# Kernel optimization log

Hardware: AMD Instinct MI355X
Metric: run time of the kernel (lower is better)

The kernel has to match this reference:

```python
import jax, jax.numpy as jnp
import numpy as np

N = 50000          # nodes
E = 1_600_000      # edges (avg degree 32)
F_IN = 48          # node features (df columns 1:-1)
H, C = 8, 8        # conv1: 8 heads x 8 channels
NC = 2             # num_classes
NEG_SLOPE = 0.2    # PyG GATConv default leaky_relu slope


def setup_inputs() -> dict:
    key = jax.random.key(0)
    ks = jax.random.split(key, 9)
    s = 0.1
    return {
        "x": jax.random.normal(ks[0], (N, F_IN), jnp.float32),
        "edge_index": jax.random.randint(ks[1], (2, E), 0, N, dtype=jnp.int64),
        "W1": jax.random.normal(ks[2], (F_IN, H * C), jnp.float32) * s,
        "att_src1": jax.random.normal(ks[3], (H, C), jnp.float32) * s,
        "att_dst1": jax.random.normal(ks[4], (H, C), jnp.float32) * s,
        "b1": jnp.zeros((H * C,), jnp.float32),
        "W2": jax.random.normal(ks[5], (H * C, NC), jnp.float32) * s,
        "att_src2": jax.random.normal(ks[6], (1, NC), jnp.float32) * s,
        "att_dst2": jax.random.normal(ks[7], (1, NC), jnp.float32) * s,
        "b2": jnp.zeros((NC,), jnp.float32),
    }


def _gat_conv(x, src, dst, W, a_src, a_dst, b, heads, out_ch, concat):
    """PyG GATConv: linear -> per-edge leaky_relu attention -> segment softmax
    over destination nodes -> scatter-sum aggregation."""
    n = x.shape[0]
    h = (x @ W).reshape(n, heads, out_ch)               # [N, H, C]
    e_src = (h * a_src).sum(-1)                          # [N, H]
    e_dst = (h * a_dst).sum(-1)                          # [N, H]
    e = jax.nn.leaky_relu(e_src[src] + e_dst[dst], NEG_SLOPE)  # [E, H]
    # numerically stable segment softmax over incoming edges of each dst node
    m = jax.ops.segment_max(e, dst, num_segments=n)      # [N, H]
    ex = jnp.exp(e - m[dst])
    den = jax.ops.segment_sum(ex, dst, num_segments=n)   # [N, H]
    alpha = ex / den[dst]                                # [E, H]
    out = jax.ops.segment_sum(h[src] * alpha[:, :, None], dst, num_segments=n)
    out = out.reshape(n, heads * out_ch) if concat else out.mean(axis=1)
    return out + b


def reference(x, edge_index, W1, att_src1, att_dst1, b1, W2, att_src2, att_dst2, b2):
    n = x.shape[0]
    loop = jnp.arange(n, dtype=edge_index.dtype)  # GATConv add_self_loops=True
    src = jnp.concatenate([edge_index[0], loop])
    dst = jnp.concatenate([edge_index[1], loop])
    h = _gat_conv(x, src, dst, W1, att_src1, att_dst1, b1, H, C, True)
    h = jax.nn.elu(h)
    out = _gat_conv(h, src, dst, W2, att_src2, att_dst2, b2, 1, NC, False)
    return jax.nn.log_softmax(out, axis=1)
```

## Files before the change

kernel.cpp:

```cpp
#include <hip/hip_runtime.h>
#include <hip/hip_bf16.h>
#include <math.h>

#define NN 50000
#define FIN 48
#define HC 64
#define NHEAD 8
#define NCH 8
#define NCLS 2
#define NEG 0.2f
#define LOG2E 1.44269504f

#define NPB 98
#define NBKT 512
#define CAP 4096
#define BCHUNK 4096
#define NR 8
#define RSH 13


__global__ void k_bin_h1(const int* __restrict__ ei, int* __restrict__ bcur,
                         int* __restrict__ pairs, int e, int tot, int nbin,
                         const float* __restrict__ x, const float* __restrict__ W1,
                         const float* __restrict__ as1, const float* __restrict__ ad1,
                         __hip_bfloat16* __restrict__ h1b, float* __restrict__ es1,
                         float* __restrict__ ed1, int n) {
    __shared__ int hist[NBKT];
    __shared__ int gbase[NBKT];
    __shared__ float Wl[FIN * HC];
    __shared__ float xs[4][FIN];
    __shared__ float hr[4][HC];
    int t = threadIdx.x;
    if ((int)blockIdx.x < nbin) {
        hist[t] = 0; hist[t + 256] = 0;
        __syncthreads();
        int base = blockIdx.x * BCHUNK;
        int end = min(base + BCHUNK, tot);
        int pk[16];
        int bp[16];
        #pragma unroll
        for (int k = 0; k < 16; ++k) {
            int i = base + t + k * 256;
            if (i < end) {
                int s, d;
                if (i < e) { s = ei[i]; d = ei[e + i]; }
                else       { s = d = i - e; }
                int b = d / NPB;
                int p = atomicAdd(&hist[b], 1);
                pk[k] = ((d - b * NPB) << 16) | s;
                bp[k] = (b << 16) | p;
            }
        }
        __syncthreads();
        for (int u = t; u < NBKT; u += 256) {
            int h = hist[u];
            gbase[u] = h ? atomicAdd(&bcur[u], h) : 0;
        }
        __syncthreads();
        #pragma unroll
        for (int k = 0; k < 16; ++k) {
            int i = base + t + k * 256;
            if (i < end) {
                int b = bp[k] >> 16;
                int p = gbase[b] + (bp[k] & 0xFFFF);
                if (p < CAP) pairs[b * CAP + p] = pk[k];
            }
        }
    } else {
        for (int i = t; i < FIN * HC; i += 256) Wl[i] = W1[i];
        int ngroups = (n + 3) >> 2;
        int nl = t >> 6, j = t & 63;
        for (int g = blockIdx.x - nbin; g < ngroups; g += gridDim.x - nbin) {
            int nb = g * 4;
            __syncthreads();
            for (int i = t; i < 4 * FIN; i += 256) {
                int l = i / FIN, k = i % FIN;
                int nd = nb + l;
                xs[l][k] = (nd < n) ? x[nd * FIN + k] : 0.f;
            }
            __syncthreads();
            float acc = 0.f;
            #pragma unroll
            for (int k = 0; k < FIN; ++k) acc += xs[nl][k] * Wl[k * HC + j];
            int nd = nb + nl;
            if (nd < n) h1b[nd * HC + j] = __float2bfloat16(acc);
            hr[nl][j] = acc;
            __syncthreads();
            if (j < 16 && nd < n) {
                int hh = j & 7;
                const float* av = (j < 8) ? as1 : ad1;
                float ev = 0.f;
                #pragma unroll
                for (int c = 0; c < NCH; ++c) ev += hr[nl][hh * NCH + c] * av[hh * NCH + c];
                ev *= LOG2E;
                if (j < 8) es1[nd * NHEAD + hh] = ev;
                else       ed1[nd * NHEAD + hh] = ev;
            }
        }
    }
}


__global__ void k_bucket_csr(const int* __restrict__ pairs, const int* __restrict__ bcur,
                             int* __restrict__ rowptr, int* __restrict__ degv,
                             int* __restrict__ csr, int n) {
    __shared__ int hist[1024];
    __shared__ int scanbuf[256];
    int b = blockIdx.x, t = threadIdx.x;
    int lo = b * NPB;
    int nn = min(NPB, n - lo);
    if (nn <= 0) return;
    int base = b * CAP;
    int cnt = min(bcur[b], CAP);
    #pragma unroll
    for (int k = 0; k < 4; ++k) hist[t + k * 256] = 0;
    __syncthreads();
    for (int i = t; i < cnt; i += 256) {
        int p = pairs[base + i];
        int key = ((p >> 16) << 3) | ((p & 0xFFFF) >> RSH);
        atomicAdd(&hist[key], 1);
    }
    __syncthreads();
    int c0 = hist[t * 4], c1 = hist[t * 4 + 1], c2 = hist[t * 4 + 2], c3 = hist[t * 4 + 3];
    int s = c0 + c1 + c2 + c3;
    scanbuf[t] = s;
    __syncthreads();
    for (int off = 1; off < 256; off <<= 1) {
        int y = (t >= off) ? scanbuf[t - off] : 0;
        __syncthreads();
        scanbuf[t] += y;
        __syncthreads();
    }
    int excl = scanbuf[t] - s;
    hist[t * 4]     = excl;
    hist[t * 4 + 1] = excl + c0;
    hist[t * 4 + 2] = excl + c0 + c1;
    hist[t * 4 + 3] = excl + c0 + c1 + c2;
    __syncthreads();
    if (t < nn) {
        int r0 = hist[t << 3];
        rowptr[lo + t] = base + r0;
        degv[lo + t] = hist[(t + 1) << 3] - r0;
    }
    __syncthreads();
    for (int i = t; i < cnt; i += 256) {
        int p = pairs[base + i];
        int key = ((p >> 16) << 3) | ((p & 0xFFFF) >> RSH);
        int pos = atomicAdd(&hist[key], 1);
        csr[base + pos] = p & 0xFFFF;
    }
}


__global__ void k_agg1(const __hip_bfloat16* __restrict__ h1b, const float* __restrict__ es1,
                       const float* __restrict__ ed1, const int* __restrict__ rowptr,
                       const int* __restrict__ degv, const int* __restrict__ csr,
                       const float* __restrict__ b1,
                       const float* __restrict__ W2, const float* __restrict__ as2,
                       const float* __restrict__ ad2, float4* __restrict__ node2, int n) {
    int wid = (blockIdx.x * blockDim.x + threadIdx.x) >> 6;
    if (wid >= n) return;
    int lane = threadIdx.x & 63;
    int j  = lane & 7;
    int hw = lane >> 3;
    int e4 = lane >> 4;
    int r  = lane & 15;
    int ha = r >> 1;
    int ch0 = (ha << 3) + ((r & 1) << 2);
    int wbase = (ha << 3) + e4;
    int start = rowptr[wid];
    int cnt = degv[wid];
    float edv = ed1[wid * NHEAD + hw];
    float sumw = 0.f;
    float a0 = 0.f, a1 = 0.f, a2 = 0.f, a3 = 0.f;
    int nbatch = cnt >> 3;

    int sl; float ev; uint2 va, vb;
    if (nbatch > 0) {
        sl = __builtin_nontemporal_load(csr + start + j);
        ev = es1[sl * NHEAD + hw];
        int su0 = __shfl(sl, e4, 64);
        int su1 = __shfl(sl, 4 + e4, 64);
        va = *(const uint2*)(h1b + su0 * HC + ch0);
        vb = *(const uint2*)(h1b + su1 * HC + ch0);
        for (int b = 1; b < nbatch; ++b) {
            int sl_n = __builtin_nontemporal_load(csr + start + b * 8 + j);
            float ev_n = es1[sl_n * NHEAD + hw];
            int su0n = __shfl(sl_n, e4, 64);
            int su1n = __shfl(sl_n, 4 + e4, 64);
            uint2 va_n = *(const uint2*)(h1b + su0n * HC + ch0);
            uint2 vb_n = *(const uint2*)(h1b + su1n * HC + ch0);
            float tt = ev + edv;
            tt = fmaxf(tt, NEG * tt);
            float w = exp2f(tt);
            sumw += w;
            float wj0 = __shfl(w, wbase, 64);
            float wj1 = __shfl(w, wbase + 4, 64);
            a0 += wj0 * __uint_as_float(va.x << 16);
            a1 += wj0 * __uint_as_float(va.x & 0xffff0000u);
            a2 += wj0 * __uint_as_float(va.y << 16);
            a3 += wj0 * __uint_as_float(va.y & 0xffff0000u);
            a0 += wj1 * __uint_as_float(vb.x << 16);
            a1 += wj1 * __uint_as_float(vb.x & 0xffff0000u);
            a2 += wj1 * __uint_as_float(vb.y << 16);
            a3 += wj1 * __uint_as_float(vb.y & 0xffff0000u);
            sl = sl_n; ev = ev_n; va = va_n; vb = vb_n;
        }
        float tt = ev + edv;
        tt = fmaxf(tt, NEG * tt);
        float w = exp2f(tt);
        sumw += w;
        float wj0 = __shfl(w, wbase, 64);
        float wj1 = __shfl(w, wbase + 4, 64);
        a0 += wj0 * __uint_as_float(va.x << 16);
        a1 += wj0 * __uint_as_float(va.x & 0xffff0000u);
        a2 += wj0 * __uint_as_float(va.y << 16);
        a3 += wj0 * __uint_as_float(va.y & 0xffff0000u);
        a0 += wj1 * __uint_as_float(vb.x << 16);
        a1 += wj1 * __uint_as_float(vb.x & 0xffff0000u);
        a2 += wj1 * __uint_as_float(vb.y << 16);
        a3 += wj1 * __uint_as_float(vb.y & 0xffff0000u);
    }
    int i = nbatch << 3;
    if (i < cnt) {
        int last = start + cnt - 1;
        int idx = start + i + j;
        int slt = csr[idx > last ? last : idx];
        float evt = es1[slt * NHEAD + hw] + edv;
        evt = fmaxf(evt, NEG * evt);
        float w = (i + j < cnt) ? exp2f(evt) : 0.f;
        sumw += w;
        #pragma unroll
        for (int it = 0; it < 2; ++it) {
            int su   = __shfl(slt, (it << 2) + e4, 64);
            float wj = __shfl(w, wbase + (it << 2), 64);
            uint2 v = *(const uint2*)(h1b + su * HC + ch0);
            a0 += wj * __uint_as_float(v.x << 16);
            a1 += wj * __uint_as_float(v.x & 0xffff0000u);
            a2 += wj * __uint_as_float(v.y << 16);
            a3 += wj * __uint_as_float(v.y & 0xffff0000u);
        }
    }
    sumw += __shfl_xor(sumw, 1, 64);
    sumw += __shfl_xor(sumw, 2, 64);
    sumw += __shfl_xor(sumw, 4, 64);
    a0 += __shfl_xor(a0, 16, 64); a0 += __shfl_xor(a0, 32, 64);
    a1 += __shfl_xor(a1, 16, 64); a1 += __shfl_xor(a1, 32, 64);
    a2 += __shfl_xor(a2, 16, 64); a2 += __shfl_xor(a2, 32, 64);
    a3 += __shfl_xor(a3, 16, 64); a3 += __shfl_xor(a3, 32, 64);
    float sden = __shfl(sumw, ha << 3, 64);
    float4 bv = *(const float4*)(b1 + ch0);
    float o0 = a0 / sden + bv.x;
    float o1 = a1 / sden + bv.y;
    float o2 = a2 / sden + bv.z;
    float o3 = a3 / sden + bv.w;
    o0 = o0 > 0.f ? o0 : expm1f(o0);
    o1 = o1 > 0.f ? o1 : expm1f(o1);
    o2 = o2 > 0.f ? o2 : expm1f(o2);
    o3 = o3 > 0.f ? o3 : expm1f(o3);
    float4 w01 = *(const float4*)(W2 + ch0 * 2);
    float4 w23 = *(const float4*)(W2 + ch0 * 2 + 4);
    float p0 = o0 * w01.x + o1 * w01.z + o2 * w23.x + o3 * w23.z;
    float p1 = o0 * w01.y + o1 * w01.w + o2 * w23.y + o3 * w23.w;
    #pragma unroll
    for (int off = 8; off > 0; off >>= 1) {
        p0 += __shfl_xor(p0, off, 64);
        p1 += __shfl_xor(p1, off, 64);
    }
    if (lane == 0) {
        float es2v = (p0 * as2[0] + p1 * as2[1]) * LOG2E;
        float ed2v = (p0 * ad2[0] + p1 * ad2[1]) * LOG2E;
        node2[wid] = make_float4(es2v, p0, p1, ed2v);
    }
}


__global__ void k_agg2(const float4* __restrict__ node2, const int* __restrict__ rowptr,
                       const int* __restrict__ degv, const int* __restrict__ csr,
                       const float* __restrict__ b2, float* __restrict__ out, int n) {
    int lane = threadIdx.x & 63;
    int wid = ((blockIdx.x * blockDim.x + threadIdx.x) >> 6) * 4 + (lane >> 4);
    if (wid >= n) return;
    int l16 = lane & 15;
    int start = rowptr[wid];
    int cnt = degv[wid];
    float edv = ((const float*)node2)[wid * 4 + 3];
    float sw = 0.f, a0 = 0.f, a1 = 0.f;
    for (int i = l16; i < cnt; i += 16) {
        int s = __builtin_nontemporal_load(csr + start + i);
        float4 t = node2[s];
        float val = t.x + edv;
        val = fmaxf(val, NEG * val);
        float w = exp2f(val);
        sw += w;
        a0 += w * t.y;
        a1 += w * t.z;
    }
    #pragma unroll
    for (int off = 8; off > 0; off >>= 1) {
        sw += __shfl_xor(sw, off, 16);
        a0 += __shfl_xor(a0, off, 16);
        a1 += __shfl_xor(a1, off, 16);
    }
    if (l16 == 0) {
        float z0 = a0 / sw + b2[0];
        float z1 = a1 / sw + b2[1];
        float mz = fmaxf(z0, z1);
        float lse = mz + logf(__expf(z0 - mz) + __expf(z1 - mz));
        out[wid * NCLS + 0] = z0 - lse;
        out[wid * NCLS + 1] = z1 - lse;
    }
}


extern "C" void kernel_launch(void* const* d_in, const int* in_sizes, int n_in,
                              void* d_out, int out_size, void* d_ws, size_t ws_size,
                              hipStream_t stream) {
    const float* x   = (const float*)d_in[0];
    const int*   ei  = (const int*)d_in[1];
    const float* W1  = (const float*)d_in[2];
    const float* as1 = (const float*)d_in[3];
    const float* ad1 = (const float*)d_in[4];
    const float* b1  = (const float*)d_in[5];
    const float* W2  = (const float*)d_in[6];
    const float* as2 = (const float*)d_in[7];
    const float* ad2 = (const float*)d_in[8];
    const float* b2  = (const float*)d_in[9];
    float* out = (float*)d_out;

    const int n = in_sizes[0] / FIN;
    const int e = in_sizes[1] / 2;
    const int tot = e + n;

    char* ws = (char*)d_ws;
    size_t off = 0;
    auto alloc = [&](size_t bytes) -> void* {
        void* p = ws + off;
        off += (bytes + 255) & ~(size_t)255;
        return p;
    };
    __hip_bfloat16* h1b = (__hip_bfloat16*)alloc((size_t)n * HC * 2);
    int* pairs   = (int*)alloc((size_t)NBKT * CAP * 4);
    int* csr     = (int*)alloc((size_t)NBKT * CAP * 4);
    float* es1   = (float*)alloc((size_t)n * NHEAD * 4);
    float* ed1   = (float*)alloc((size_t)n * NHEAD * 4);
    float4* node2 = (float4*)alloc((size_t)n * 16);
    int* rowptr  = (int*)alloc((size_t)n * 4);
    int* degv    = (int*)alloc((size_t)n * 4);
    int* bcur    = (int*)alloc(NBKT * 4);

    const int nbin = (tot + BCHUNK - 1) / BCHUNK;

    hipMemsetAsync(bcur, 0, NBKT * 4, stream);
    k_bin_h1<<<nbin + 1024, 256, 0, stream>>>(ei, bcur, pairs, e, tot, nbin,
                                              x, W1, as1, ad1, h1b, es1, ed1, n);
    k_bucket_csr<<<NBKT, 256, 0, stream>>>(pairs, bcur, rowptr, degv, csr, n);
    k_agg1<<<(n * 64 + 255) / 256, 256, 0, stream>>>(h1b, es1, ed1, rowptr, degv, csr,
                                                     b1, W2, as2, ad2, node2, n);
    k_agg2<<<(n * 16 + 255) / 256, 256, 0, stream>>>(node2, rowptr, degv, csr, b2, out, n);
}
```

Measured before the change: 121.6 us.

## Store source attention scores in bf16 and simplify bucket CSR build

Source-side attention logits are now stored as bf16, halving the bytes of the per-edge gathered es1 reads in the layer-1 aggregation. The lane mapping in k_agg1 is transposed so that 8 adjacent lanes read the 8 heads of one source node contiguously, with shuffle indices and reductions adjusted to match. The CSR bucket kernel drops the sub-keyed (source-range) ordering and builds a plain per-destination histogram, keeping pairs in registers so the pairs buffer is read once instead of twice. The cost is reduced precision in the attention logits and the loss of source-sorted neighbor order within each row, which may hurt gather locality.

```diff
diff --git a/kernel.cpp b/kernel.cpp
--- a/kernel.cpp
+++ b/kernel.cpp
@@ -15,15 +15,13 @@
 #define NBKT 512
 #define CAP 4096
 #define BCHUNK 4096
-#define NR 8
-#define RSH 13
 
 
 __global__ void k_bin_h1(const int* __restrict__ ei, int* __restrict__ bcur,
                          int* __restrict__ pairs, int e, int tot, int nbin,
                          const float* __restrict__ x, const float* __restrict__ W1,
                          const float* __restrict__ as1, const float* __restrict__ ad1,
-                         __hip_bfloat16* __restrict__ h1b, float* __restrict__ es1,
+                         __hip_bfloat16* __restrict__ h1b, __hip_bfloat16* __restrict__ es1b,
                          float* __restrict__ ed1, int n) {
     __shared__ int hist[NBKT];
     __shared__ int gbase[NBKT];
@@ -93,7 +91,7 @@
                 #pragma unroll
                 for (int c = 0; c < NCH; ++c) ev += hr[nl][hh * NCH + c] * av[hh * NCH + c];
                 ev *= LOG2E;
-                if (j < 8) es1[nd * NHEAD + hh] = ev;
+                if (j < 8) es1b[nd * NHEAD + hh] = __float2bfloat16(ev);
                 else       ed1[nd * NHEAD + hh] = ev;
             }
         }
@@ -104,55 +102,53 @@
 __global__ void k_bucket_csr(const int* __restrict__ pairs, const int* __restrict__ bcur,
                              int* __restrict__ rowptr, int* __restrict__ degv,
                              int* __restrict__ csr, int n) {
-    __shared__ int hist[1024];
-    __shared__ int scanbuf[256];
+    __shared__ int hist[256];
     int b = blockIdx.x, t = threadIdx.x;
     int lo = b * NPB;
     int nn = min(NPB, n - lo);
     if (nn <= 0) return;
     int base = b * CAP;
     int cnt = min(bcur[b], CAP);
+    hist[t] = 0;
+    __syncthreads();
+    int srcv[16];
+    int kp[16];
     #pragma unroll
-    for (int k = 0; k < 4; ++k) hist[t + k * 256] = 0;
+    for (int k = 0; k < 16; ++k) {
+        int i = t + k * 256;
+        if (i < cnt) {
+            int p = pairs[base + i];
+            int key = p >> 16;
+            int pos = atomicAdd(&hist[key], 1);
+            srcv[k] = p & 0xFFFF;
+            kp[k] = (key << 16) | pos;
+        }
+    }
     __syncthreads();
-    for (int i = t; i < cnt; i += 256) {
-        int p = pairs[base + i];
-        int key = ((p >> 16) << 3) | ((p & 0xFFFF) >> RSH);
-        atomicAdd(&hist[key], 1);
-    }
+    int v = hist[t];
+    for (int off = 1; off < 256; off <<= 1) {
+        int y = (t >= off) ? hist[t - off] : 0;
+        __syncthreads();
+        hist[t] += y;
+        __syncthreads();
+    }
+    int excl = hist[t] - v;
+    if (t < nn) { rowptr[lo + t] = base + excl; degv[lo + t] = v; }
     __syncthreads();
-    int c0 = hist[t * 4], c1 = hist[t * 4 + 1], c2 = hist[t * 4 + 2], c3 = hist[t * 4 + 3];
-    int s = c0 + c1 + c2 + c3;
-    scanbuf[t] = s;
+    hist[t] = excl;
     __syncthreads();
-    for (int off = 1; off < 256; off <<= 1) {
-        int y = (t >= off) ? scanbuf[t - off] : 0;
-        __syncthreads();
-        scanbuf[t] += y;
-        __syncthreads();
-    }
-    int excl = scanbuf[t] - s;
-    hist[t * 4]     = excl;
-    hist[t * 4 + 1] = excl + c0;
-    hist[t * 4 + 2] = excl + c0 + c1;
-    hist[t * 4 + 3] = excl + c0 + c1 + c2;
-    __syncthreads();
-    if (t < nn) {
-        int r0 = hist[t << 3];
-        rowptr[lo + t] = base + r0;
-        degv[lo + t] = hist[(t + 1) << 3] - r0;
-    }
-    __syncthreads();
-    for (int i = t; i < cnt; i += 256) {
-        int p = pairs[base + i];
-        int key = ((p >> 16) << 3) | ((p & 0xFFFF) >> RSH);
-        int pos = atomicAdd(&hist[key], 1);
-        csr[base + pos] = p & 0xFFFF;
-    }
-}
-
-
-__global__ void k_agg1(const __hip_bfloat16* __restrict__ h1b, const float* __restrict__ es1,
+    #pragma unroll
+    for (int k = 0; k < 16; ++k) {
+        int i = t + k * 256;
+        if (i < cnt) {
+            int key = kp[k] >> 16, pos = kp[k] & 0xFFFF;
+            csr[base + hist[key] + pos] = srcv[k];
+        }
+    }
+}
+
+
+__global__ void k_agg1(const __hip_bfloat16* __restrict__ h1b, const __hip_bfloat16* __restrict__ es1b,
                        const float* __restrict__ ed1, const int* __restrict__ rowptr,
                        const int* __restrict__ degv, const int* __restrict__ csr,
                        const float* __restrict__ b1,
@@ -161,13 +157,13 @@
     int wid = (blockIdx.x * blockDim.x + threadIdx.x) >> 6;
     if (wid >= n) return;
     int lane = threadIdx.x & 63;
-    int j  = lane & 7;
-    int hw = lane >> 3;
+    int j  = lane >> 3;
+    int hw = lane & 7;
     int e4 = lane >> 4;
     int r  = lane & 15;
     int ha = r >> 1;
     int ch0 = (ha << 3) + ((r & 1) << 2);
-    int wbase = (ha << 3) + e4;
+    int wbase = (e4 << 3) + ha;
     int start = rowptr[wid];
     int cnt = degv[wid];
     float edv = ed1[wid * NHEAD + hw];
@@ -178,16 +174,16 @@
     int sl; float ev; uint2 va, vb;
     if (nbatch > 0) {
         sl = __builtin_nontemporal_load(csr + start + j);
-        ev = es1[sl * NHEAD + hw];
-        int su0 = __shfl(sl, e4, 64);
-        int su1 = __shfl(sl, 4 + e4, 64);
+        ev = __bfloat162float(es1b[sl * NHEAD + hw]);
+        int su0 = __shfl(sl, e4 << 3, 64);
+        int su1 = __shfl(sl, (4 + e4) << 3, 64);
         va = *(const uint2*)(h1b + su0 * HC + ch0);
         vb = *(const uint2*)(h1b + su1 * HC + ch0);
         for (int b = 1; b < nbatch; ++b) {
             int sl_n = __builtin_nontemporal_load(csr + start + b * 8 + j);
-            float ev_n = es1[sl_n * NHEAD + hw];
-            int su0n = __shfl(sl_n, e4, 64);
-            int su1n = __shfl(sl_n, 4 + e4, 64);
+            float ev_n = __bfloat162float(es1b[sl_n * NHEAD + hw]);
+            int su0n = __shfl(sl_n, e4 << 3, 64);
+            int su1n = __shfl(sl_n, (4 + e4) << 3, 64);
             uint2 va_n = *(const uint2*)(h1b + su0n * HC + ch0);
             uint2 vb_n = *(const uint2*)(h1b + su1n * HC + ch0);
             float tt = ev + edv;
@@ -195,7 +191,7 @@
             float w = exp2f(tt);
             sumw += w;
             float wj0 = __shfl(w, wbase, 64);
-            float wj1 = __shfl(w, wbase + 4, 64);
+            float wj1 = __shfl(w, wbase + 32, 64);
             a0 += wj0 * __uint_as_float(va.x << 16);
             a1 += wj0 * __uint_as_float(va.x & 0xffff0000u);
             a2 += wj0 * __uint_as_float(va.y << 16);
@@ -211,7 +207,7 @@
         float w = exp2f(tt);
         sumw += w;
         float wj0 = __shfl(w, wbase, 64);
-        float wj1 = __shfl(w, wbase + 4, 64);
+        float wj1 = __shfl(w, wbase + 32, 64);
         a0 += wj0 * __uint_as_float(va.x << 16);
         a1 += wj0 * __uint_as_float(va.x & 0xffff0000u);
         a2 += wj0 * __uint_as_float(va.y << 16);
@@ -226,14 +222,14 @@
         int last = start + cnt - 1;
         int idx = start + i + j;
         int slt = csr[idx > last ? last : idx];
-        float evt = es1[slt * NHEAD + hw] + edv;
+        float evt = __bfloat162float(es1b[slt * NHEAD + hw]) + edv;
         evt = fmaxf(evt, NEG * evt);
         float w = (i + j < cnt) ? exp2f(evt) : 0.f;
         sumw += w;
         #pragma unroll
         for (int it = 0; it < 2; ++it) {
-            int su   = __shfl(slt, (it << 2) + e4, 64);
-            float wj = __shfl(w, wbase + (it << 2), 64);
+            int su   = __shfl(slt, ((it << 2) + e4) << 3, 64);
+            float wj = __shfl(w, wbase + (it << 5), 64);
             uint2 v = *(const uint2*)(h1b + su * HC + ch0);
             a0 += wj * __uint_as_float(v.x << 16);
             a1 += wj * __uint_as_float(v.x & 0xffff0000u);
@@ -241,14 +237,14 @@
             a3 += wj * __uint_as_float(v.y & 0xffff0000u);
         }
     }
-    sumw += __shfl_xor(sumw, 1, 64);
-    sumw += __shfl_xor(sumw, 2, 64);
-    sumw += __shfl_xor(sumw, 4, 64);
+    sumw += __shfl_xor(sumw, 8, 64);
+    sumw += __shfl_xor(sumw, 16, 64);
+    sumw += __shfl_xor(sumw, 32, 64);
     a0 += __shfl_xor(a0, 16, 64); a0 += __shfl_xor(a0, 32, 64);
     a1 += __shfl_xor(a1, 16, 64); a1 += __shfl_xor(a1, 32, 64);
     a2 += __shfl_xor(a2, 16, 64); a2 += __shfl_xor(a2, 32, 64);
     a3 += __shfl_xor(a3, 16, 64); a3 += __shfl_xor(a3, 32, 64);
-    float sden = __shfl(sumw, ha << 3, 64);
+    float sden = __shfl(sumw, ha, 64);
     float4 bv = *(const float4*)(b1 + ch0);
     float o0 = a0 / sden + bv.x;
     float o1 = a1 / sden + bv.y;
@@ -339,10 +335,10 @@
         off += (bytes + 255) & ~(size_t)255;
         return p;
     };
-    __hip_bfloat16* h1b = (__hip_bfloat16*)alloc((size_t)n * HC * 2);
+    __hip_bfloat16* h1b  = (__hip_bfloat16*)alloc((size_t)n * HC * 2);
+    __hip_bfloat16* es1b = (__hip_bfloat16*)alloc((size_t)n * NHEAD * 2);
     int* pairs   = (int*)alloc((size_t)NBKT * CAP * 4);
     int* csr     = (int*)alloc((size_t)NBKT * CAP * 4);
-    float* es1   = (float*)alloc((size_t)n * NHEAD * 4);
     float* ed1   = (float*)alloc((size_t)n * NHEAD * 4);
     float4* node2 = (float4*)alloc((size_t)n * 16);
     int* rowptr  = (int*)alloc((size_t)n * 4);
@@ -353,9 +349,9 @@
 
     hipMemsetAsync(bcur, 0, NBKT * 4, stream);
     k_bin_h1<<<nbin + 1024, 256, 0, stream>>>(ei, bcur, pairs, e, tot, nbin,
-                                              x, W1, as1, ad1, h1b, es1, ed1, n);
+                                              x, W1, as1, ad1, h1b, es1b, ed1, n);
     k_bucket_csr<<<NBKT, 256, 0, stream>>>(pairs, bcur, rowptr, degv, csr, n);
-    k_agg1<<<(n * 64 + 255) / 256, 256, 0, stream>>>(h1b, es1, ed1, rowptr, degv, csr,
+    k_agg1<<<(n * 64 + 255) / 256, 256, 0, stream>>>(h1b, es1b, ed1, rowptr, degv, csr,
                                                      b1, W2, as2, ad2, node2, n);
     k_agg2<<<(n * 16 + 255) / 256, 256, 0, stream>>>(node2, rowptr, degv, csr, b2, out, n);
 }
```

After: 121.2 us. About the same (-0.3%).
